# Performance work log

Hardware: AMD Instinct MI355X
Metric: run time of the kernel (lower is better)

Reference implementation:

```python
import jax, jax.numpy as jnp
import numpy as np

B, S, D, H = 64, 256, 1024, 1024
F0, F1 = 1024, 1024
STDV = 1.0 / np.sqrt(H)


def setup_inputs() -> dict:
    key = jax.random.key(0)
    ks = jax.random.split(key, 14)
    u = lambda k, shape: jax.random.uniform(k, shape, jnp.float32, -STDV, STDV)
    return {
        "input_feats": jax.random.normal(ks[0], (B, S, D), jnp.float32),
        "feat0": jax.random.normal(ks[1], (B, S, F0), jnp.float32),
        "feat1": jax.random.normal(ks[2], (B, S, F1), jnp.float32),
        "weight_ih": u(ks[3], (3 * H, D)),
        "weight_hh": u(ks[4], (3 * H, H)),
        "weight_fh0": u(ks[5], (2 * H, F0)),
        "weight_fh1": u(ks[6], (2 * H, F1)),
        "bias_ih": u(ks[7], (3 * H,)),
        "bias_hh": u(ks[8], (3 * H,)),
        "bias_fh0": u(ks[9], (2 * H,)),
        "bias_fh1": u(ks[10], (2 * H,)),
    }


def reference(input_feats, feat0, feat1, weight_ih, weight_hh, weight_fh0,
              weight_fh1, bias_ih, bias_hh, bias_fh0, bias_fh1):
    hid = weight_hh.shape[1]
    # Input-to-gate and feature-to-gate projections have no recurrence:
    # batch them over all timesteps up front (same math as per-step F.linear).
    gi = input_feats @ weight_ih.T + bias_ih                      # [B,S,3H]
    gf = (feat0 @ weight_fh0.T + feat1 @ weight_fh1.T
          + bias_fh0 + bias_fh1)                                  # [B,S,2H]
    gi_t = jnp.swapaxes(gi, 0, 1)                                 # [S,B,3H]
    gf_t = jnp.swapaxes(gf, 0, 1)                                 # [S,B,2H]

    def step(hx, xs):
        gi_s, gf_s = xs
        gh = hx @ weight_hh.T + bias_hh                           # [B,3H]
        i_r, i_i, i_n = jnp.split(gi_s, 3, axis=1)
        h_r, h_i, h_n = jnp.split(gh, 3, axis=1)
        f_r, f_i = jnp.split(gf_s, 2, axis=1)
        resetgate = jax.nn.sigmoid(i_r + h_r + f_r)
        inputgate = jax.nn.sigmoid(i_i + h_i + f_i)
        newgate = jnp.tanh(i_n + resetgate * h_n)
        hy = newgate + inputgate * (hx - newgate)
        return hy, hy

    h0 = jnp.zeros((input_feats.shape[0], hid), input_feats.dtype)
    h_last, ys = jax.lax.scan(step, h0, (gi_t, gf_t))
    output = jnp.swapaxes(ys, 0, 1)                               # [B,S,H]
    return output, h_last
```

## Files before the change

### kernel.cpp

```cpp
#include <hip/hip_runtime.h>

typedef unsigned short u16;
typedef __attribute__((ext_vector_type(8))) short short8;
typedef __attribute__((ext_vector_type(4))) short short4v;
typedef __attribute__((ext_vector_type(4))) float f32x4;

#define BB 64
#define SS 256
#define HH 1024
#define NG 3072
#define KK 1024
#define NOUT ((size_t)BB * SS * HH)

#define OFF_GSUM 0ull
#define OFF_HB0 100663296ull
#define OFF_HB1 100794368ull
#define OFF_BAR 100925440ull
#define OFF_FLAG 100925504ull
#define WS_NEED 100925568ull

__device__ __forceinline__ float bf2f(u16 x) {
  unsigned u = ((unsigned)x) << 16;
  float f;
  __builtin_memcpy(&f, &u, 4);
  return f;
}
__device__ __forceinline__ float bf2f_u(unsigned x) {
  unsigned u = x << 16;
  float f;
  __builtin_memcpy(&f, &u, 4);
  return f;
}
__device__ __forceinline__ u16 f2bf(float f) {
  unsigned u;
  __builtin_memcpy(&u, &f, 4);
  u = (u + 0x7fffu + ((u >> 16) & 1u)) >> 16;
  return (u16)u;
}
template <int F32>
__device__ __forceinline__ float ldval(const void* p, size_t i) {
  return F32 ? ((const float*)p)[i] : bf2f(((const u16*)p)[i]);
}
__device__ __forceinline__ float sigmoidf_(float x) {
  return __builtin_amdgcn_rcpf(1.f + __expf(-x));
}
__device__ __forceinline__ float tanhf_(float x) {
  return 2.f * __builtin_amdgcn_rcpf(1.f + __expf(-2.f * x)) - 1.f;
}

typedef const __attribute__((address_space(1))) void* gcptr;
typedef __attribute__((address_space(3))) void* lptr;

__global__ void detect_kernel(const u16* __restrict__ w, unsigned* __restrict__ flag) {
  if (threadIdx.x == 0 && blockIdx.x == 0) {
    int hi = 0;
    for (int i = 0; i < 256; ++i) hi += (((w[i] >> 7) & 0xFF) >= 128) ? 1 : 0;
    *flag = (hi > 16) ? 1u : 0u;
  }
}

template <int F32>
__global__ __launch_bounds__(256) void gemm_fused(
    const void* __restrict__ Xv, const void* __restrict__ F0v, const void* __restrict__ F1v,
    const void* __restrict__ Wihv, const void* __restrict__ Wf0v, const void* __restrict__ Wf1v,
    const void* __restrict__ bihv, const void* __restrict__ bf0v, const void* __restrict__ bf1v,
    u16* __restrict__ C, const unsigned* __restrict__ flag) {
  if ((*flag != 0u) != (F32 != 0)) return;
  __shared__ __align__(16) u16 ldsA[128 * 32];
  __shared__ __align__(16) u16 ldsB[128 * 32];
  const int t = threadIdx.x;
  const int nwg = gridDim.x;
  const int cpx = nwg >> 3;
  const int wg = (blockIdx.x & 7) * cpx + (blockIdx.x >> 3);
  const int ntn = NG / 128;
  const int m0 = (wg / ntn) * 128;
  const int n0 = (wg % ntn) * 128;
  const int lane = t & 63, wv = t >> 6;
  const int wm = wv >> 1, wn = wv & 1;

  f32x4 acc[4][4] = {};

  const int fi0 = t, fi1 = t + 256;
  const int r0 = fi0 >> 2, c0 = (fi0 & 3) * 8;
  const int r1 = fi1 >> 2, c1 = (fi1 & 3) * 8;

  const int nsrc = (n0 < 2048) ? 3 : 1;
  for (int src = 0; src < nsrc; ++src) {
    const void* Ap = (src == 0) ? Xv : ((src == 1) ? F0v : F1v);
    const void* Wp = (src == 0) ? Wihv : ((src == 1) ? Wf0v : Wf1v);
    for (int k0 = 0; k0 < KK; k0 += 32) {
      if (F32) {
        const float* Af = (const float*)Ap + (size_t)m0 * KK;
        const float* Wf = (const float*)Wp + (size_t)n0 * KK;
#pragma unroll
        for (int it = 0; it < 4; ++it) {
          int idx = t + it * 256;
          int r = idx >> 3, q = idx & 7;
          f32x4 va = *(const f32x4*)(Af + (size_t)r * KK + k0 + q * 4);
          f32x4 vb = *(const f32x4*)(Wf + (size_t)r * KK + k0 + q * 4);
          short4v sa, sb;
#pragma unroll
          for (int j = 0; j < 4; ++j) { sa[j] = (short)f2bf(va[j]); sb[j] = (short)f2bf(vb[j]); }
          *(short4v*)&ldsA[r * 32 + q * 4] = sa;
          *(short4v*)&ldsB[r * 32 + q * 4] = sb;
        }
      } else {
        const u16* Ab = (const u16*)Ap + (size_t)m0 * KK;
        const u16* Wb = (const u16*)Wp + (size_t)n0 * KK;
        __builtin_amdgcn_global_load_lds((gcptr)(Ab + (size_t)r0 * KK + k0 + c0), (lptr)(&ldsA[fi0 * 8]), 16, 0, 0);
        __builtin_amdgcn_global_load_lds((gcptr)(Ab + (size_t)r1 * KK + k0 + c1), (lptr)(&ldsA[fi1 * 8]), 16, 0, 0);
        __builtin_amdgcn_global_load_lds((gcptr)(Wb + (size_t)r0 * KK + k0 + c0), (lptr)(&ldsB[fi0 * 8]), 16, 0, 0);
        __builtin_amdgcn_global_load_lds((gcptr)(Wb + (size_t)r1 * KK + k0 + c1), (lptr)(&ldsB[fi1 * 8]), 16, 0, 0);
      }
      __syncthreads();
      short8 af[4], bw[4];
#pragma unroll
      for (int i = 0; i < 4; ++i) {
        af[i] = *(const short8*)&ldsA[(wm * 64 + i * 16 + (lane & 15)) * 32 + (lane >> 4) * 8];
        bw[i] = *(const short8*)&ldsB[(wn * 64 + i * 16 + (lane & 15)) * 32 + (lane >> 4) * 8];
      }
#pragma unroll
      for (int i = 0; i < 4; ++i)
#pragma unroll
        for (int j = 0; j < 4; ++j)
          acc[i][j] = __builtin_amdgcn_mfma_f32_16x16x32_bf16(af[i], bw[j], acc[i][j], 0, 0, 0);
      __syncthreads();
    }
  }
#pragma unroll
  for (int j = 0; j < 4; ++j) {
    const int col = n0 + wn * 64 + j * 16 + (lane & 15);
    float bias = ldval<F32>(bihv, (size_t)col);
    if (col < 2048) bias += ldval<F32>(bf0v, (size_t)col) + ldval<F32>(bf1v, (size_t)col);
#pragma unroll
    for (int i = 0; i < 4; ++i) {
      const int row = m0 + wm * 64 + i * 16 + (lane >> 4) * 4;
#pragma unroll
      for (int r = 0; r < 4; ++r)
        C[(size_t)(row + r) * NG + col] = f2bf(acc[i][j][r] + bias);
    }
  }
}

#define SB0() __builtin_amdgcn_sched_barrier(0)

#define ISSUE8(buf, bkk)                                                        \
  _Pragma("unroll")                                                             \
  for (int i_ = 0; i_ < 8; ++i_)                                                \
    asm volatile("global_load_dwordx4 %0, %1, off sc0 sc1"                      \
                 : "=v"(buf[i_]) : "v"(ap + ((bkk) + i_) * 32));

#define CONSUME8(buf, bkk)                                                      \
  _Pragma("unroll")                                                             \
  for (int i_ = 0; i_ < 8; ++i_) {                                              \
    const int ko_ = ((bkk) + i_) * 64 + kb;                                     \
    short8 br_ = *(const short8*)(s0 + (ko_ ^ sw));                             \
    short8 bj_ = *(const short8*)(s1 + (ko_ ^ sw));                             \
    short8 bn_ = *(const short8*)(s2 + (ko_ ^ sw));                             \
    ar = __builtin_amdgcn_mfma_f32_16x16x32_bf16(buf[i_], br_, ar, 0, 0, 0);    \
    ai = __builtin_amdgcn_mfma_f32_16x16x32_bf16(buf[i_], bj_, ai, 0, 0, 0);    \
    an = __builtin_amdgcn_mfma_f32_16x16x32_bf16(buf[i_], bn_, an, 0, 0, 0);    \
  }

#define ISSUE_GSUM(snext)                                                       \
  _Pragma("unroll")                                                             \
  for (int r_ = 0; r_ < 4; ++r_) {                                              \
    const u16* gp_ = gsum + ((size_t)(mb + quad * 4 + r_) * 256 + (size_t)(snext)) * 3072 + jl; \
    asm volatile("global_load_ushort %0, %1, off" : "=v"(pgu[r_ * 3 + 0]) : "v"(gp_));          \
    asm volatile("global_load_ushort %0, %1, off" : "=v"(pgu[r_ * 3 + 1]) : "v"(gp_ + 1024));   \
    asm volatile("global_load_ushort %0, %1, off" : "=v"(pgu[r_ * 3 + 2]) : "v"(gp_ + 2048));   \
  }

template <int F32>
__global__ __launch_bounds__(256, 1) void scan_kernel(
    const u16* __restrict__ gsum, const void* __restrict__ Whhv, const void* __restrict__ bhhv,
    u16* __restrict__ h0buf, u16* __restrict__ h1buf,
    void* __restrict__ outv, unsigned* __restrict__ bar, const unsigned* __restrict__ flag) {
  if ((*flag != 0u) != (F32 != 0)) return;
  extern __shared__ u16 wlds[];
  const int t = threadIdx.x, w = blockIdx.x;
  const int j0 = w * 16;
  for (int c = t; c < 48 * 128; c += 256) {
    int q = c >> 7, chunk = c & 127;
    int g = q >> 4, i = q & 15;
    short8 v;
    if (F32) {
      const float* wf = (const float*)Whhv + ((size_t)(g * 1024 + j0 + i)) * 1024 + chunk * 8;
      f32x4 a = *(const f32x4*)wf, b = *(const f32x4*)(wf + 4);
#pragma unroll
      for (int j = 0; j < 4; ++j) { v[j] = (short)f2bf(a[j]); v[4 + j] = (short)f2bf(b[j]); }
    } else {
      v = *(const short8*)((const u16*)Whhv + ((size_t)(g * 1024 + j0 + i)) * 1024 + chunk * 8);
    }
    *(short8*)((char*)wlds + q * 2048 + ((chunk * 16) ^ (i << 4))) = v;
  }
  const int lane = t & 63;
  const int bi = lane & 15;
  const int quad = lane >> 4;
  const int jl = j0 + bi;
  const int mb = (t >> 6) * 16;
  const float bhr = ldval<F32>(bhhv, (size_t)jl);
  const float bhi = ldval<F32>(bhhv, (size_t)(1024 + jl));
  const float bhn = ldval<F32>(bhhv, (size_t)(2048 + jl));
  __syncthreads();

  float hreg[4] = {0.f, 0.f, 0.f, 0.f};

  const int kb = quad * 16;
  const int sw = bi << 4;
  const char* wbytes = (const char*)wlds;
  const char* s0 = wbytes + (size_t)(0 + bi) * 2048;
  const char* s1 = wbytes + (size_t)(16 + bi) * 2048;
  const char* s2 = wbytes + (size_t)(32 + bi) * 2048;

  unsigned pgu[12];
  ISSUE_GSUM(0);
  asm volatile("s_waitcnt vmcnt(0)" ::: "memory");
  SB0();

  short8 aA[8], aB[8], aC[8], aD[8];
  for (int s = 0; s < 256; ++s) {
    f32x4 ar = {0.f, 0.f, 0.f, 0.f};
    f32x4 ai = {0.f, 0.f, 0.f, 0.f};
    f32x4 an = {0.f, 0.f, 0.f, 0.f};
    if (s > 0) {
      asm volatile("s_waitcnt vmcnt(24)" ::: "memory");
      SB0();
      CONSUME8(aA, 0);
      asm volatile("s_waitcnt vmcnt(16)" ::: "memory");
      SB0();
      CONSUME8(aB, 8);
      asm volatile("s_waitcnt vmcnt(8)" ::: "memory");
      SB0();
      CONSUME8(aC, 16);
      asm volatile("s_waitcnt vmcnt(0)" ::: "memory");
      SB0();
      CONSUME8(aD, 24);
      SB0();
    }
    u16* hw = (s & 1) ? h0buf : h1buf;
#pragma unroll
    for (int r = 0; r < 4; ++r) {
      int b = mb + quad * 4 + r;
      size_t m = (size_t)b * 256 + s;
      float rg = sigmoidf_(bf2f_u(pgu[r * 3 + 0]) + ar[r] + bhr);
      float ig = sigmoidf_(bf2f_u(pgu[r * 3 + 1]) + ai[r] + bhi);
      float ng = tanhf_(bf2f_u(pgu[r * 3 + 2]) + rg * (an[r] + bhn));
      float hy = ng + ig * (hreg[r] - ng);
      hreg[r] = hy;
      unsigned hv = (unsigned)f2bf(hy);
      if (s < 255) {
        asm volatile("global_store_short %0, %1, off sc0 sc1"
                     :: "v"(hw + (size_t)b * 1024 + jl), "v"(hv) : "memory");
      }
      if (F32) {
        float hyv = hy;
        asm volatile("global_store_dword %0, %1, off nt"
                     :: "v"((float*)outv + m * 1024 + jl), "v"(hyv) : "memory");
      } else {
        asm volatile("global_store_short %0, %1, off nt"
                     :: "v"((u16*)outv + m * 1024 + jl), "v"(hv) : "memory");
      }
    }
    if (s < 255) {
      ISSUE_GSUM(s + 1);
      asm volatile("s_waitcnt vmcnt(16)" ::: "memory");
      SB0();
      __builtin_amdgcn_s_barrier();
      if (t == 0) {
        unsigned one = 1;
        asm volatile("global_atomic_add %0, %1, off" :: "v"(bar), "v"(one) : "memory");
        unsigned v;
        do {
          __builtin_amdgcn_s_sleep(1);
          asm volatile("global_load_dword %0, %1, off sc0 sc1\n\ts_waitcnt vmcnt(0)"
                       : "=v"(v) : "v"(bar) : "memory");
        } while (v < (unsigned)(64 * (s + 1)));
      }
      __builtin_amdgcn_s_barrier();
      const u16* hcur = (s & 1) ? h0buf : h1buf;
      const u16* ap = hcur + (size_t)(mb + bi) * 1024 + quad * 8;
      SB0();
      ISSUE8(aA, 0);
      ISSUE8(aB, 8);
      ISSUE8(aC, 16);
      ISSUE8(aD, 24);
      SB0();
    }
  }
#pragma unroll
  for (int r = 0; r < 4; ++r) {
    int b = mb + quad * 4 + r;
    if (F32) ((float*)outv)[NOUT + (size_t)b * 1024 + jl] = hreg[r];
    else     ((u16*)outv)[NOUT + (size_t)b * 1024 + jl] = f2bf(hreg[r]);
  }
}

extern "C" void kernel_launch(void* const* d_in, const int* in_sizes, int n_in,
                              void* d_out, int out_size, void* d_ws, size_t ws_size,
                              hipStream_t stream) {
  if (ws_size < WS_NEED) return;
  const void* x   = d_in[0];
  const void* f0  = d_in[1];
  const void* f1  = d_in[2];
  const void* wih = d_in[3];
  const void* whh = d_in[4];
  const void* wf0 = d_in[5];
  const void* wf1 = d_in[6];
  const void* bih = d_in[7];
  const void* bhh = d_in[8];
  const void* bf0 = d_in[9];
  const void* bf1 = d_in[10];

  char* ws = (char*)d_ws;
  u16* gsum = (u16*)(ws + OFF_GSUM);
  u16* hb0 = (u16*)(ws + OFF_HB0);
  u16* hb1 = (u16*)(ws + OFF_HB1);
  unsigned* bar = (unsigned*)(ws + OFF_BAR);
  unsigned* flag = (unsigned*)(ws + OFF_FLAG);

  hipMemsetAsync(bar, 0, 128, stream);
  hipMemsetAsync(hb0, 0, 131072, stream);
  hipMemsetAsync(hb1, 0, 131072, stream);

  detect_kernel<<<dim3(1), dim3(64), 0, stream>>>((const u16*)wih, flag);

  gemm_fused<0><<<dim3(3072), dim3(256), 0, stream>>>(x, f0, f1, wih, wf0, wf1, bih, bf0, bf1, gsum, flag);
  gemm_fused<1><<<dim3(3072), dim3(256), 0, stream>>>(x, f0, f1, wih, wf0, wf1, bih, bf0, bf1, gsum, flag);

  hipFuncSetAttribute(reinterpret_cast<const void*>(&scan_kernel<0>),
                      hipFuncAttributeMaxDynamicSharedMemorySize, 98304);
  hipFuncSetAttribute(reinterpret_cast<const void*>(&scan_kernel<1>),
                      hipFuncAttributeMaxDynamicSharedMemorySize, 98304);
  scan_kernel<0><<<dim3(64), dim3(256), 98304, stream>>>(gsum, whh, bhh, hb0, hb1, d_out, bar, flag);
  scan_kernel<1><<<dim3(64), dim3(256), 98304, stream>>>(gsum, whh, bhh, hb0, hb1, d_out, bar, flag);
}
```

Before: 2.516 ms.

## Drop dtype detection, load fp32 tiles directly to LDS and convert in-register

```diff
diff --git a/kernel.cpp b/kernel.cpp
--- a/kernel.cpp
+++ b/kernel.cpp
@@ -2,7 +2,6 @@
 
 typedef unsigned short u16;
 typedef __attribute__((ext_vector_type(8))) short short8;
-typedef __attribute__((ext_vector_type(4))) short short4v;
 typedef __attribute__((ext_vector_type(4))) float f32x4;
 
 #define BB 64
@@ -16,15 +15,8 @@
 #define OFF_HB0 100663296ull
 #define OFF_HB1 100794368ull
 #define OFF_BAR 100925440ull
-#define OFF_FLAG 100925504ull
 #define WS_NEED 100925568ull
 
-__device__ __forceinline__ float bf2f(u16 x) {
-  unsigned u = ((unsigned)x) << 16;
-  float f;
-  __builtin_memcpy(&f, &u, 4);
-  return f;
-}
 __device__ __forceinline__ float bf2f_u(unsigned x) {
   unsigned u = x << 16;
   float f;
@@ -37,9 +29,13 @@
   u = (u + 0x7fffu + ((u >> 16) & 1u)) >> 16;
   return (u16)u;
 }
-template <int F32>
-__device__ __forceinline__ float ldval(const void* p, size_t i) {
-  return F32 ? ((const float*)p)[i] : bf2f(((const u16*)p)[i]);
+__device__ __forceinline__ short8 cvt8(f32x4 lo, f32x4 hi) {
+  union { unsigned u[4]; short8 s; } r;
+  asm("v_cvt_pk_bf16_f32 %0, %1, %2" : "=v"(r.u[0]) : "v"(lo[0]), "v"(lo[1]));
+  asm("v_cvt_pk_bf16_f32 %0, %1, %2" : "=v"(r.u[1]) : "v"(lo[2]), "v"(lo[3]));
+  asm("v_cvt_pk_bf16_f32 %0, %1, %2" : "=v"(r.u[2]) : "v"(hi[0]), "v"(hi[1]));
+  asm("v_cvt_pk_bf16_f32 %0, %1, %2" : "=v"(r.u[3]) : "v"(hi[2]), "v"(hi[3]));
+  return r.s;
 }
 __device__ __forceinline__ float sigmoidf_(float x) {
   return __builtin_amdgcn_rcpf(1.f + __expf(-x));
@@ -51,23 +47,13 @@
 typedef const __attribute__((address_space(1))) void* gcptr;
 typedef __attribute__((address_space(3))) void* lptr;
 
-__global__ void detect_kernel(const u16* __restrict__ w, unsigned* __restrict__ flag) {
-  if (threadIdx.x == 0 && blockIdx.x == 0) {
-    int hi = 0;
-    for (int i = 0; i < 256; ++i) hi += (((w[i] >> 7) & 0xFF) >= 128) ? 1 : 0;
-    *flag = (hi > 16) ? 1u : 0u;
-  }
-}
-
-template <int F32>
 __global__ __launch_bounds__(256) void gemm_fused(
-    const void* __restrict__ Xv, const void* __restrict__ F0v, const void* __restrict__ F1v,
-    const void* __restrict__ Wihv, const void* __restrict__ Wf0v, const void* __restrict__ Wf1v,
-    const void* __restrict__ bihv, const void* __restrict__ bf0v, const void* __restrict__ bf1v,
-    u16* __restrict__ C, const unsigned* __restrict__ flag) {
-  if ((*flag != 0u) != (F32 != 0)) return;
-  __shared__ __align__(16) u16 ldsA[128 * 32];
-  __shared__ __align__(16) u16 ldsB[128 * 32];
+    const float* __restrict__ X, const float* __restrict__ F0, const float* __restrict__ F1,
+    const float* __restrict__ Wih, const float* __restrict__ Wf0, const float* __restrict__ Wf1,
+    const float* __restrict__ bih, const float* __restrict__ bf0, const float* __restrict__ bf1,
+    u16* __restrict__ C) {
+  __shared__ __align__(16) float ldsA[128 * 32];
+  __shared__ __align__(16) float ldsB[128 * 32];
   const int t = threadIdx.x;
   const int nwg = gridDim.x;
   const int cpx = nwg >> 3;
@@ -80,44 +66,42 @@
 
   f32x4 acc[4][4] = {};
 
-  const int fi0 = t, fi1 = t + 256;
-  const int r0 = fi0 >> 2, c0 = (fi0 & 3) * 8;
-  const int r1 = fi1 >> 2, c1 = (fi1 & 3) * 8;
-
   const int nsrc = (n0 < 2048) ? 3 : 1;
   for (int src = 0; src < nsrc; ++src) {
-    const void* Ap = (src == 0) ? Xv : ((src == 1) ? F0v : F1v);
-    const void* Wp = (src == 0) ? Wihv : ((src == 1) ? Wf0v : Wf1v);
+    const float* Ap = (src == 0) ? X : ((src == 1) ? F0 : F1);
+    const float* Wp = (src == 0) ? Wih : ((src == 1) ? Wf0 : Wf1);
+    const float* Abase = Ap + (size_t)m0 * KK;
+    const float* Wbase = Wp + (size_t)n0 * KK;
     for (int k0 = 0; k0 < KK; k0 += 32) {
-      if (F32) {
-        const float* Af = (const float*)Ap + (size_t)m0 * KK;
-        const float* Wf = (const float*)Wp + (size_t)n0 * KK;
-#pragma unroll
-        for (int it = 0; it < 4; ++it) {
-          int idx = t + it * 256;
-          int r = idx >> 3, q = idx & 7;
-          f32x4 va = *(const f32x4*)(Af + (size_t)r * KK + k0 + q * 4);
-          f32x4 vb = *(const f32x4*)(Wf + (size_t)r * KK + k0 + q * 4);
-          short4v sa, sb;
-#pragma unroll
-          for (int j = 0; j < 4; ++j) { sa[j] = (short)f2bf(va[j]); sb[j] = (short)f2bf(vb[j]); }
-          *(short4v*)&ldsA[r * 32 + q * 4] = sa;
-          *(short4v*)&ldsB[r * 32 + q * 4] = sb;
-        }
-      } else {
-        const u16* Ab = (const u16*)Ap + (size_t)m0 * KK;
-        const u16* Wb = (const u16*)Wp + (size_t)n0 * KK;
-        __builtin_amdgcn_global_load_lds((gcptr)(Ab + (size_t)r0 * KK + k0 + c0), (lptr)(&ldsA[fi0 * 8]), 16, 0, 0);
-        __builtin_amdgcn_global_load_lds((gcptr)(Ab + (size_t)r1 * KK + k0 + c1), (lptr)(&ldsA[fi1 * 8]), 16, 0, 0);
-        __builtin_amdgcn_global_load_lds((gcptr)(Wb + (size_t)r0 * KK + k0 + c0), (lptr)(&ldsB[fi0 * 8]), 16, 0, 0);
-        __builtin_amdgcn_global_load_lds((gcptr)(Wb + (size_t)r1 * KK + k0 + c1), (lptr)(&ldsB[fi1 * 8]), 16, 0, 0);
+#pragma unroll
+      for (int c = 0; c < 4; ++c) {
+        const int idx = c * 256 + t;
+        const int row = idx >> 3, q = idx & 7;
+        const int qs = q ^ (row & 7);
+        __builtin_amdgcn_global_load_lds((gcptr)(Abase + (size_t)row * KK + k0 + qs * 4),
+                                         (lptr)(&ldsA[idx * 4]), 16, 0, 0);
+        __builtin_amdgcn_global_load_lds((gcptr)(Wbase + (size_t)row * KK + k0 + qs * 4),
+                                         (lptr)(&ldsB[idx * 4]), 16, 0, 0);
       }
       __syncthreads();
       short8 af[4], bw[4];
+      const int g0 = (lane >> 4) * 2;
 #pragma unroll
       for (int i = 0; i < 4; ++i) {
-        af[i] = *(const short8*)&ldsA[(wm * 64 + i * 16 + (lane & 15)) * 32 + (lane >> 4) * 8];
-        bw[i] = *(const short8*)&ldsB[(wn * 64 + i * 16 + (lane & 15)) * 32 + (lane >> 4) * 8];
+        {
+          const int row = wm * 64 + i * 16 + (lane & 15);
+          const int ga = g0 ^ (row & 7), gb = (g0 + 1) ^ (row & 7);
+          f32x4 lo = *(const f32x4*)&ldsA[row * 32 + ga * 4];
+          f32x4 hi = *(const f32x4*)&ldsA[row * 32 + gb * 4];
+          af[i] = cvt8(lo, hi);
+        }
+        {
+          const int row = wn * 64 + i * 16 + (lane & 15);
+          const int ga = g0 ^ (row & 7), gb = (g0 + 1) ^ (row & 7);
+          f32x4 lo = *(const f32x4*)&ldsB[row * 32 + ga * 4];
+          f32x4 hi = *(const f32x4*)&ldsB[row * 32 + gb * 4];
+          bw[i] = cvt8(lo, hi);
+        }
       }
 #pragma unroll
       for (int i = 0; i < 4; ++i)
@@ -130,8 +114,8 @@
 #pragma unroll
   for (int j = 0; j < 4; ++j) {
     const int col = n0 + wn * 64 + j * 16 + (lane & 15);
-    float bias = ldval<F32>(bihv, (size_t)col);
-    if (col < 2048) bias += ldval<F32>(bf0v, (size_t)col) + ldval<F32>(bf1v, (size_t)col);
+    float bias = bih[col];
+    if (col < 2048) bias += bf0[col] + bf1[col];
 #pragma unroll
     for (int i = 0; i < 4; ++i) {
       const int row = m0 + wm * 64 + i * 16 + (lane >> 4) * 4;
@@ -147,7 +131,7 @@
 #define ISSUE8(buf, bkk)                                                        \
   _Pragma("unroll")                                                             \
   for (int i_ = 0; i_ < 8; ++i_)                                                \
-    asm volatile("global_load_dwordx4 %0, %1, off sc0 sc1"                      \
+    asm volatile("global_load_dwordx4 %0, %1, off"                              \
                  : "=v"(buf[i_]) : "v"(ap + ((bkk) + i_) * 32));
 
 #define CONSUME8(buf, bkk)                                                      \
@@ -171,27 +155,18 @@
     asm volatile("global_load_ushort %0, %1, off" : "=v"(pgu[r_ * 3 + 2]) : "v"(gp_ + 2048));   \
   }
 
-template <int F32>
 __global__ __launch_bounds__(256, 1) void scan_kernel(
-    const u16* __restrict__ gsum, const void* __restrict__ Whhv, const void* __restrict__ bhhv,
+    const u16* __restrict__ gsum, const float* __restrict__ Whh, const float* __restrict__ bhh,
     u16* __restrict__ h0buf, u16* __restrict__ h1buf,
-    void* __restrict__ outv, unsigned* __restrict__ bar, const unsigned* __restrict__ flag) {
-  if ((*flag != 0u) != (F32 != 0)) return;
+    float* __restrict__ out, unsigned* __restrict__ bar) {
   extern __shared__ u16 wlds[];
   const int t = threadIdx.x, w = blockIdx.x;
   const int j0 = w * 16;
   for (int c = t; c < 48 * 128; c += 256) {
     int q = c >> 7, chunk = c & 127;
     int g = q >> 4, i = q & 15;
-    short8 v;
-    if (F32) {
-      const float* wf = (const float*)Whhv + ((size_t)(g * 1024 + j0 + i)) * 1024 + chunk * 8;
-      f32x4 a = *(const f32x4*)wf, b = *(const f32x4*)(wf + 4);
-#pragma unroll
-      for (int j = 0; j < 4; ++j) { v[j] = (short)f2bf(a[j]); v[4 + j] = (short)f2bf(b[j]); }
-    } else {
-      v = *(const short8*)((const u16*)Whhv + ((size_t)(g * 1024 + j0 + i)) * 1024 + chunk * 8);
-    }
+    const float* wf = Whh + ((size_t)(g * 1024 + j0 + i)) * 1024 + chunk * 8;
+    short8 v = cvt8(*(const f32x4*)wf, *(const f32x4*)(wf + 4));
     *(short8*)((char*)wlds + q * 2048 + ((chunk * 16) ^ (i << 4))) = v;
   }
   const int lane = t & 63;
@@ -199,9 +174,9 @@
   const int quad = lane >> 4;
   const int jl = j0 + bi;
   const int mb = (t >> 6) * 16;
-  const float bhr = ldval<F32>(bhhv, (size_t)jl);
-  const float bhi = ldval<F32>(bhhv, (size_t)(1024 + jl));
-  const float bhn = ldval<F32>(bhhv, (size_t)(2048 + jl));
+  const float bhr = bhh[jl];
+  const float bhi = bhh[1024 + jl];
+  const float bhn = bhh[2048 + jl];
   __syncthreads();
 
   float hreg[4] = {0.f, 0.f, 0.f, 0.f};
@@ -239,28 +214,32 @@
       SB0();
     }
     u16* hw = (s & 1) ? h0buf : h1buf;
+    float hy4[4];
+    unsigned hv4[4];
 #pragma unroll
     for (int r = 0; r < 4; ++r) {
-      int b = mb + quad * 4 + r;
-      size_t m = (size_t)b * 256 + s;
       float rg = sigmoidf_(bf2f_u(pgu[r * 3 + 0]) + ar[r] + bhr);
       float ig = sigmoidf_(bf2f_u(pgu[r * 3 + 1]) + ai[r] + bhi);
       float ng = tanhf_(bf2f_u(pgu[r * 3 + 2]) + rg * (an[r] + bhn));
       float hy = ng + ig * (hreg[r] - ng);
       hreg[r] = hy;
-      unsigned hv = (unsigned)f2bf(hy);
-      if (s < 255) {
+      hy4[r] = hy;
+      hv4[r] = (unsigned)f2bf(hy);
+    }
+    if (s < 255) {
+#pragma unroll
+      for (int r = 0; r < 4; ++r) {
+        int b = mb + quad * 4 + r;
         asm volatile("global_store_short %0, %1, off sc0 sc1"
-                     :: "v"(hw + (size_t)b * 1024 + jl), "v"(hv) : "memory");
+                     :: "v"(hw + (size_t)b * 1024 + jl), "v"(hv4[r]) : "memory");
       }
-      if (F32) {
-        float hyv = hy;
-        asm volatile("global_store_dword %0, %1, off nt"
-                     :: "v"((float*)outv + m * 1024 + jl), "v"(hyv) : "memory");
-      } else {
-        asm volatile("global_store_short %0, %1, off nt"
-                     :: "v"((u16*)outv + m * 1024 + jl), "v"(hv) : "memory");
-      }
+    }
+#pragma unroll
+    for (int r = 0; r < 4; ++r) {
+      int b = mb + quad * 4 + r;
+      size_t m = (size_t)b * 256 + s;
+      asm volatile("global_store_dword %0, %1, off sc0 sc1"
+                   :: "v"(out + m * 1024 + jl), "v"(hy4[r]) : "memory");
     }
     if (s < 255) {
       ISSUE_GSUM(s + 1);
@@ -271,16 +250,19 @@
         unsigned one = 1;
         asm volatile("global_atomic_add %0, %1, off" :: "v"(bar), "v"(one) : "memory");
         unsigned v;
-        do {
-          __builtin_amdgcn_s_sleep(1);
+        for (;;) {
           asm volatile("global_load_dword %0, %1, off sc0 sc1\n\ts_waitcnt vmcnt(0)"
                        : "=v"(v) : "v"(bar) : "memory");
-        } while (v < (unsigned)(64 * (s + 1)));
+          if (v >= (unsigned)(64 * (s + 1))) break;
+          __builtin_amdgcn_s_sleep(1);
+        }
       }
       __builtin_amdgcn_s_barrier();
+      SB0();
+      __builtin_amdgcn_fence(__ATOMIC_ACQUIRE, "agent");
+      SB0();
       const u16* hcur = (s & 1) ? h0buf : h1buf;
       const u16* ap = hcur + (size_t)(mb + bi) * 1024 + quad * 8;
-      SB0();
       ISSUE8(aA, 0);
       ISSUE8(aB, 8);
       ISSUE8(aC, 16);
@@ -291,8 +273,7 @@
 #pragma unroll
   for (int r = 0; r < 4; ++r) {
     int b = mb + quad * 4 + r;
-    if (F32) ((float*)outv)[NOUT + (size_t)b * 1024 + jl] = hreg[r];
-    else     ((u16*)outv)[NOUT + (size_t)b * 1024 + jl] = f2bf(hreg[r]);
+    out[NOUT + (size_t)b * 1024 + jl] = hreg[r];
   }
 }
 
@@ -300,38 +281,31 @@
                               void* d_out, int out_size, void* d_ws, size_t ws_size,
                               hipStream_t stream) {
   if (ws_size < WS_NEED) return;
-  const void* x   = d_in[0];
-  const void* f0  = d_in[1];
-  const void* f1  = d_in[2];
-  const void* wih = d_in[3];
-  const void* whh = d_in[4];
-  const void* wf0 = d_in[5];
-  const void* wf1 = d_in[6];
-  const void* bih = d_in[7];
-  const void* bhh = d_in[8];
-  const void* bf0 = d_in[9];
-  const void* bf1 = d_in[10];
+  const float* x   = (const float*)d_in[0];
+  const float* f0  = (const float*)d_in[1];
+  const float* f1  = (const float*)d_in[2];
+  const float* wih = (const float*)d_in[3];
+  const float* whh = (const float*)d_in[4];
+  const float* wf0 = (const float*)d_in[5];
+  const float* wf1 = (const float*)d_in[6];
+  const float* bih = (const float*)d_in[7];
+  const float* bhh = (const float*)d_in[8];
+  const float* bf0 = (const float*)d_in[9];
+  const float* bf1 = (const float*)d_in[10];
 
   char* ws = (char*)d_ws;
   u16* gsum = (u16*)(ws + OFF_GSUM);
   u16* hb0 = (u16*)(ws + OFF_HB0);
   u16* hb1 = (u16*)(ws + OFF_HB1);
   unsigned* bar = (unsigned*)(ws + OFF_BAR);
-  unsigned* flag = (unsigned*)(ws + OFF_FLAG);
 
   hipMemsetAsync(bar, 0, 128, stream);
   hipMemsetAsync(hb0, 0, 131072, stream);
   hipMemsetAsync(hb1, 0, 131072, stream);
 
-  detect_kernel<<<dim3(1), dim3(64), 0, stream>>>((const u16*)wih, flag);
-
-  gemm_fused<0><<<dim3(3072), dim3(256), 0, stream>>>(x, f0, f1, wih, wf0, wf1, bih, bf0, bf1, gsum, flag);
-  gemm_fused<1><<<dim3(3072), dim3(256), 0, stream>>>(x, f0, f1, wih, wf0, wf1, bih, bf0, bf1, gsum, flag);
-
-  hipFuncSetAttribute(reinterpret_cast<const void*>(&scan_kernel<0>),
+  gemm_fused<<<dim3(3072), dim3(256), 0, stream>>>(x, f0, f1, wih, wf0, wf1, bih, bf0, bf1, gsum);
+
+  hipFuncSetAttribute(reinterpret_cast<const void*>(&scan_kernel),
                       hipFuncAttributeMaxDynamicSharedMemorySize, 98304);
-  hipFuncSetAttribute(reinterpret_cast<const void*>(&scan_kernel<1>),
-                      hipFuncAttributeMaxDynamicSharedMemorySize, 98304);
-  scan_kernel<0><<<dim3(64), dim3(256), 98304, stream>>>(gsum, whh, bhh, hb0, hb1, d_out, bar, flag);
-  scan_kernel<1><<<dim3(64), dim3(256), 98304, stream>>>(gsum, whh, bhh, hb0, hb1, d_out, bar, flag);
-}
+  scan_kernel<<<dim3(64), dim3(256), 98304, stream>>>(gsum, whh, bhh, hb0, hb1, (float*)d_out, bar);
+}
```

Measured after the change: 2.916 ms. 1.16x slower.
